# Kernel optimization log

Measured on AMD Instinct MI355X. Metric: run time of the kernel, lower is better.

## Reference

```python
import jax, jax.numpy as jnp
import numpy as np

ETA = 1.0
C_STAB = 0.1
SIGMA2 = 512.0  # RBF bandwidth, kernel_args['sigma2']
N_SAMPLE, S, D = 8192, 64, 512


def rbf_kernel(x, sigma2):
    # K[i,j] = exp(-||x_i - x_j||^2 / (2*sigma2)); x: [n, d] -> K: [n, n]
    sq = jnp.sum(x * x, axis=1)
    d2 = sq[:, None] + sq[None, :] - 2.0 * (x @ x.T)
    return jnp.exp(-d2 / (2.0 * sigma2))


def setup_inputs() -> dict:
    key = jax.random.key(0)
    k1, k2, k3 = jax.random.split(key, 3)
    return {
        "input_data": jax.random.normal(k1, (N_SAMPLE, D), dtype=jnp.float32),
        "weight": jax.random.normal(k2, (N_SAMPLE, S), dtype=jnp.float32),
        "inv_lambda_diag": jax.random.normal(k3, (S,), dtype=jnp.float32),
    }


def reference(input_data, weight, inv_lambda_diag):
    K = rbf_kernel(input_data, SIGMA2)          # [n, n]
    E = weight.T @ K                             # [s, n] : e_j for all samples at once
    # loss1 = sum_i e_i^T diag(inv_lambda) e_i, scaled
    loss1 = -jnp.sum(inv_lambda_diag[:, None] * E * E) / (2.0 * ETA ** 2)
    # loss2 = trace(W^T K W) = sum_{s,n} E[s,n] * W[n,s]
    loss2 = jnp.einsum("sn,ns->", E, weight) / (2.0 * ETA)
    L = loss1 + loss2
    return L + (C_STAB / 2.0) * jnp.square(L)
```

## Files before the change

### kernel.cpp

```cpp
#include <hip/hip_runtime.h>
#include <hip/hip_bf16.h>

typedef __bf16 bf16x8 __attribute__((ext_vector_type(8)));
typedef float f32x4 __attribute__((ext_vector_type(4)));
typedef long longx2 __attribute__((ext_vector_type(2)));
typedef int i32x8 __attribute__((ext_vector_type(8)));

#define N 8192
#define D 512
#define NS 64

#define XS_OFF 0
#define WT_OFF (4 * 1024 * 1024)
#define SQ_OFF (WT_OFF + 1024 * 1024)
#define EP_OFF (SQ_OFF + 32 * 1024)
#define SC_OFF (EP_OFF + 8 * 64 * 8192 * 4)

#define BAR() do { asm volatile("s_waitcnt lgkmcnt(0)" ::: "memory"); \
                   __builtin_amdgcn_s_barrier(); } while (0)

__global__ __launch_bounds__(256) void prep(const float* __restrict__ X,
                                            const float* __restrict__ W,
                                            unsigned char* __restrict__ Xs,
                                            float* __restrict__ sq,
                                            __bf16* __restrict__ WTs,
                                            float* __restrict__ Sacc) {
    __shared__ float T[64][65];
    int t = threadIdx.x;
    if (blockIdx.x == 0 && t == 0) {
        Sacc[0] = 0.f; Sacc[1] = 0.f; ((int*)Sacc)[2] = 0;
    }
    if (blockIdx.x < 2048) {
        int row = blockIdx.x * 4 + (t >> 6);
        int l = t & 63;
        const float* src = X + (size_t)row * D + l * 8;
        float4 v0 = *(const float4*)src;
        float4 v1 = *(const float4*)(src + 4);
        int w0 = __builtin_amdgcn_cvt_pk_fp8_f32(v0.x, v0.y, 0, false);
        w0     = __builtin_amdgcn_cvt_pk_fp8_f32(v0.z, v0.w, w0, true);
        int w1 = __builtin_amdgcn_cvt_pk_fp8_f32(v1.x, v1.y, 0, false);
        w1     = __builtin_amdgcn_cvt_pk_fp8_f32(v1.z, v1.w, w1, true);
        uint2 pk = make_uint2((unsigned)w0, (unsigned)w1);
        *(uint2*)(Xs + (size_t)row * 512 + l * 8) = pk;
        float acc = v0.x*v0.x + v0.y*v0.y + v0.z*v0.z + v0.w*v0.w
                  + v1.x*v1.x + v1.y*v1.y + v1.z*v1.z + v1.w*v1.w;
        for (int off = 32; off > 0; off >>= 1) acc += __shfl_down(acc, off);
        if (l == 0) sq[row] = acc;
    } else {
        int i0 = (blockIdx.x - 2048) * 64;
        for (int j = 0; j < 16; ++j) {
            int idx = t + 256 * j;
            T[idx & 63][idx >> 6] = W[(size_t)(i0 + (idx >> 6)) * NS + (idx & 63)];
        }
        __syncthreads();
        for (int h = 0; h < 2; ++h)
            for (int j = 0; j < 8; ++j) {
                int idx = t + 256 * j;
                int s = idx >> 5, il = idx & 31;
                WTs[(size_t)((i0 >> 5) + h) * 2048 + idx] = (__bf16)T[s][h * 32 + il];
            }
    }
}

__global__ __launch_bounds__(256, 2) void kpca_main(
        const unsigned char* __restrict__ Xs, const __bf16* __restrict__ WTs,
        const float* __restrict__ sq, float* __restrict__ Ep) {
    __shared__ __align__(16) unsigned char XiKT[18432];
    __shared__ __align__(16) unsigned char XnHi[3 * 16384];
    unsigned char* Xi = XiKT;
    __bf16* KT = (__bf16*)XiKT;

    const int t = threadIdx.x;
    const int w = t >> 6, l = t & 63;
    const int quad = l >> 4, l15 = l & 15;
    const int wm = w >> 1, wn = w & 1;
    const int n0 = blockIdx.x * 128;
    const int ic0 = blockIdx.y * 1024;

    union U8 { longx2 h[2]; i32x8 v; };

    U8 bc[4];
    {
        const unsigned char* Bb = Xs + (size_t)(n0 + wn * 64 + l15) * 512 + quad * 32;
        #pragma unroll
        for (int nt = 0; nt < 4; ++nt) {
            bc[nt].h[0] = *(const longx2*)(Bb + nt * 8192);
            bc[nt].h[1] = *(const longx2*)(Bb + nt * 8192 + 16);
        }
    }
    #pragma unroll 4
    for (int m = 0; m < 12; ++m) {
        int id = m * 256 + t;
        int c = id >> 10, rem = id & 1023;
        int r = rem >> 3, j = rem & 7;
        uint4 v = *(const uint4*)(Xs + (size_t)(n0 + r) * 512 + 128 + c * 128 + j * 16);
        *(uint4*)(XnHi + c * 16384 + r * 128 + ((j ^ (r & 7)) << 4)) = v;
    }
    float sqn_v[4];
    #pragma unroll
    for (int nt = 0; nt < 4; ++nt)
        sqn_v[nt] = sq[n0 + wn * 64 + nt * 16 + l15];

    f32x4 accE[4][2];
    #pragma unroll
    for (int st = 0; st < 4; ++st)
        for (int n2 = 0; n2 < 2; ++n2)
            accE[st][n2] = (f32x4){0.f, 0.f, 0.f, 0.f};

    const int rB = t >> 3;
    const int cB = (t & 7) * 16;
    const int swoff = (((t & 7) ^ ((t >> 3) & 7)) << 4);

    const int oswL = (((2 * quad)     ^ (l15 & 7)) << 4);
    const int oswH = (((2 * quad + 1) ^ (l15 & 7)) << 4);

    {
        const unsigned char* g = Xs + (size_t)(ic0 + rB) * 512 + cB;
        #pragma unroll
        for (int j = 0; j < 4; ++j)
            *(uint4*)(Xi + (size_t)(j * 32 + rB) * 128 + swoff) =
                *(const uint4*)(g + (size_t)j * 32 * 512);
    }

    uint4 q[4];

    for (int it = 0; it < 8; ++it) {
        const int i0 = ic0 + it * 128;
        f32x4 accG[4][4];
        #pragma unroll
        for (int mt = 0; mt < 4; ++mt)
            for (int nt = 0; nt < 4; ++nt)
                accG[mt][nt] = (f32x4){0.f, 0.f, 0.f, 0.f};

        if (it > 0) {
            BAR();
            #pragma unroll
            for (int j = 0; j < 4; ++j)
                *(uint4*)(Xi + (size_t)(j * 32 + rB) * 128 + swoff) = q[j];
        }

        #pragma unroll
        for (int ks = 0; ks < 4; ++ks) {
            if (ks < 3) {
                const unsigned char* g =
                    Xs + (size_t)(ic0 + it * 128 + rB) * 512 + (ks + 1) * 128 + cB;
                #pragma unroll
                for (int j = 0; j < 4; ++j)
                    q[j] = *(const uint4*)(g + (size_t)j * 32 * 512);
            }
            BAR();

            U8 a[4];
            const unsigned char* abase = Xi + (wm * 64 + l15) * 128;
            #pragma unroll
            for (int mt = 0; mt < 4; ++mt) {
                a[mt].h[0] = *(const longx2*)(abase + mt * 2048 + oswL);
                a[mt].h[1] = *(const longx2*)(abase + mt * 2048 + oswH);
            }
            __builtin_amdgcn_s_setprio(1);
            if (ks == 0) {
                #pragma unroll
                for (int nt = 0; nt < 4; ++nt)
                    #pragma unroll
                    for (int mt = 0; mt < 4; ++mt)
                        accG[mt][nt] = __builtin_amdgcn_mfma_scale_f32_16x16x128_f8f6f4(
                            a[mt].v, bc[nt].v, accG[mt][nt],
                            0, 0, 0, 0x7F7F7F7F, 0, 0x7F7F7F7F);
            } else {
                const unsigned char* bbase =
                    XnHi + (ks - 1) * 16384 + (wn * 64 + l15) * 128;
                #pragma unroll
                for (int nt = 0; nt < 4; ++nt) {
                    U8 bb;
                    bb.h[0] = *(const longx2*)(bbase + nt * 2048 + oswL);
                    bb.h[1] = *(const longx2*)(bbase + nt * 2048 + oswH);
                    #pragma unroll
                    for (int mt = 0; mt < 4; ++mt)
                        accG[mt][nt] = __builtin_amdgcn_mfma_scale_f32_16x16x128_f8f6f4(
                            a[mt].v, bb.v, accG[mt][nt],
                            0, 0, 0, 0x7F7F7F7F, 0, 0x7F7F7F7F);
                }
            }
            __builtin_amdgcn_s_setprio(0);

            if (ks < 3) {
                BAR();
                #pragma unroll
                for (int j = 0; j < 4; ++j)
                    *(uint4*)(Xi + (size_t)(j * 32 + rB) * 128 + swoff) = q[j];
            }
        }

        const __bf16* wslab = WTs + (size_t)(i0 >> 5) * 2048;

        auto write_pk = [&]() {
            #pragma unroll
            for (int mt = 0; mt < 4; ++mt) {
                f32x4 si = *(const f32x4*)(sq + i0 + wm * 64 + mt * 16 + quad * 4);
                #pragma unroll
                for (int nt = 0; nt < 4; ++nt) {
                    float sn = sqn_v[nt];
                    union { __bf16 h[4]; uint2 u; } u;
                    #pragma unroll
                    for (int r = 0; r < 4; ++r) {
                        float d2 = si[r] + sn - 2.0f * accG[mt][nt][r];
                        u.h[r] = (__bf16)__expf(d2 * -9.765625e-4f);
                    }
                    *(uint2*)(KT + (wn * 64 + nt * 16 + l15) * 72 + mt * 16 + quad * 4)
                        = u.u;
                }
            }
        };

        bf16x8 aw[2][4];
        #pragma unroll
        for (int kc2 = 0; kc2 < 2; ++kc2)
            for (int st = 0; st < 4; ++st)
                aw[kc2][st] = *(const bf16x8*)(wslab + kc2 * 2048 +
                                               (st * 16 + l15) * 32 + quad * 8);

        BAR();
        if (wm == 0) write_pk();
        BAR();
        #pragma unroll
        for (int kc2 = 0; kc2 < 2; ++kc2) {
            bf16x8 bk[2];
            for (int n2 = 0; n2 < 2; ++n2)
                bk[n2] = *(const bf16x8*)(KT + (w * 32 + n2 * 16 + l15) * 72 +
                                          kc2 * 32 + quad * 8);
            #pragma unroll
            for (int st = 0; st < 4; ++st)
                for (int n2 = 0; n2 < 2; ++n2)
                    accE[st][n2] = __builtin_amdgcn_mfma_f32_16x16x32_bf16(
                        aw[kc2][st], bk[n2], accE[st][n2], 0, 0, 0);
        }
        #pragma unroll
        for (int kc2 = 0; kc2 < 2; ++kc2)
            for (int st = 0; st < 4; ++st)
                aw[kc2][st] = *(const bf16x8*)(wslab + (kc2 + 2) * 2048 +
                                               (st * 16 + l15) * 32 + quad * 8);
        BAR();
        if (wm == 1) write_pk();
        if (it < 7) {
            const unsigned char* g =
                Xs + (size_t)(ic0 + (it + 1) * 128 + rB) * 512 + cB;
            #pragma unroll
            for (int j = 0; j < 4; ++j)
                q[j] = *(const uint4*)(g + (size_t)j * 32 * 512);
        }
        BAR();
        #pragma unroll
        for (int kc2 = 0; kc2 < 2; ++kc2) {
            bf16x8 bk[2];
            for (int n2 = 0; n2 < 2; ++n2)
                bk[n2] = *(const bf16x8*)(KT + (w * 32 + n2 * 16 + l15) * 72 +
                                          kc2 * 32 + quad * 8);
            #pragma unroll
            for (int st = 0; st < 4; ++st)
                for (int n2 = 0; n2 < 2; ++n2)
                    accE[st][n2] = __builtin_amdgcn_mfma_f32_16x16x32_bf16(
                        aw[kc2][st], bk[n2], accE[st][n2], 0, 0, 0);
        }
    }

    float* ep = Ep + (size_t)blockIdx.y * (NS * N);
    #pragma unroll
    for (int st = 0; st < 4; ++st)
        for (int n2 = 0; n2 < 2; ++n2)
            for (int r = 0; r < 4; ++r) {
                int s = st * 16 + quad * 4 + r;
                int n = n0 + w * 32 + n2 * 16 + l15;
                ep[(size_t)s * N + n] = accE[st][n2][r];
            }
}

__global__ __launch_bounds__(256) void loss_kernel(const float* __restrict__ Ep,
                                                   const __bf16* __restrict__ WTs,
                                                   const float* __restrict__ lam,
                                                   float* __restrict__ Sacc,
                                                   float* __restrict__ out) {
    int s = blockIdx.x >> 2;
    int nb = (blockIdx.x & 3) * 2048;
    int t = threadIdx.x;
    float a1 = 0.f, a2 = 0.f;
    for (int j = 0; j < 8; ++j) {
        int n = nb + t + j * 256;
        float e = 0.f;
        #pragma unroll
        for (int c = 0; c < 8; ++c)
            e += Ep[(size_t)c * (NS * N) + (size_t)s * N + n];
        a1 += e * e;
        a2 += e * (float)WTs[(size_t)(n >> 5) * 2048 + s * 32 + (n & 31)];
    }
    for (int off = 32; off > 0; off >>= 1) {
        a1 += __shfl_down(a1, off);
        a2 += __shfl_down(a2, off);
    }
    __shared__ float r1[4], r2[4];
    int wv = t >> 6, ln = t & 63;
    if (ln == 0) { r1[wv] = a1; r2[wv] = a2; }
    __syncthreads();
    if (t == 0) {
        atomicAdd(Sacc + 0, lam[s] * (r1[0] + r1[1] + r1[2] + r1[3]));
        atomicAdd(Sacc + 1, r2[0] + r2[1] + r2[2] + r2[3]);
        __threadfence();
        int prev = atomicAdd((int*)Sacc + 2, 1);
        if (prev == 255) {
            __threadfence();
            volatile float* vs = (volatile float*)Sacc;
            float L = 0.5f * (vs[1] - vs[0]);
            out[0] = L + 0.05f * L * L;
        }
    }
}

extern "C" void kernel_launch(void* const* d_in, const int* in_sizes, int n_in,
                              void* d_out, int out_size, void* d_ws, size_t ws_size,
                              hipStream_t stream) {
    const float* X   = (const float*)d_in[0];
    const float* W   = (const float*)d_in[1];
    const float* lam = (const float*)d_in[2];
    float* out = (float*)d_out;
    char* ws = (char*)d_ws;
    unsigned char* Xs = (unsigned char*)(ws + XS_OFF);
    __bf16* WTs = (__bf16*)(ws + WT_OFF);
    float* sq   = (float*)(ws + SQ_OFF);
    float* Ep   = (float*)(ws + EP_OFF);
    float* Sacc = (float*)(ws + SC_OFF);

    prep<<<2048 + 128, 256, 0, stream>>>(X, W, Xs, sq, WTs, Sacc);
    kpca_main<<<dim3(64, 8), 256, 0, stream>>>(Xs, WTs, sq, Ep);
    loss_kernel<<<256, 256, 0, stream>>>(Ep, WTs, lam, Sacc, out);
}
```

Baseline: 173.2 us.

## Stage full Xn tile in LDS and XOR-swizzle the K tile layout

The first 128-byte K-chunk of the Xn tile now goes to shared memory together with the other three, instead of being held in registers (bc). All four k-steps then share one code path. The bf16 K tile moves from a padded 72-element row stride to a 128-byte row with an XOR swizzle. This frees registers and aims to reduce LDS bank conflicts on the K writes and reads. In exchange, LDS use grows from about 66KB to 80KB per block, which may limit occupancy at two blocks per CU.

After: 165.4 us. 1.05x faster.

```diff
diff --git a/kernel.cpp b/kernel.cpp
--- a/kernel.cpp
+++ b/kernel.cpp
@@ -65,10 +65,9 @@
 __global__ __launch_bounds__(256, 2) void kpca_main(
         const unsigned char* __restrict__ Xs, const __bf16* __restrict__ WTs,
         const float* __restrict__ sq, float* __restrict__ Ep) {
-    __shared__ __align__(16) unsigned char XiKT[18432];
-    __shared__ __align__(16) unsigned char XnHi[3 * 16384];
+    __shared__ __align__(16) unsigned char XiKT[16384];
+    __shared__ __align__(16) unsigned char XnHi[4 * 16384];
     unsigned char* Xi = XiKT;
-    __bf16* KT = (__bf16*)XiKT;
 
     const int t = threadIdx.x;
     const int w = t >> 6, l = t & 63;
@@ -76,24 +75,16 @@
     const int wm = w >> 1, wn = w & 1;
     const int n0 = blockIdx.x * 128;
     const int ic0 = blockIdx.y * 1024;
+    const int sw7 = l15 & 7;
 
     union U8 { longx2 h[2]; i32x8 v; };
 
-    U8 bc[4];
-    {
-        const unsigned char* Bb = Xs + (size_t)(n0 + wn * 64 + l15) * 512 + quad * 32;
-        #pragma unroll
-        for (int nt = 0; nt < 4; ++nt) {
-            bc[nt].h[0] = *(const longx2*)(Bb + nt * 8192);
-            bc[nt].h[1] = *(const longx2*)(Bb + nt * 8192 + 16);
-        }
-    }
     #pragma unroll 4
-    for (int m = 0; m < 12; ++m) {
+    for (int m = 0; m < 16; ++m) {
         int id = m * 256 + t;
         int c = id >> 10, rem = id & 1023;
         int r = rem >> 3, j = rem & 7;
-        uint4 v = *(const uint4*)(Xs + (size_t)(n0 + r) * 512 + 128 + c * 128 + j * 16);
+        uint4 v = *(const uint4*)(Xs + (size_t)(n0 + r) * 512 + c * 128 + j * 16);
         *(uint4*)(XnHi + c * 16384 + r * 128 + ((j ^ (r & 7)) << 4)) = v;
     }
     float sqn_v[4];
@@ -111,8 +102,8 @@
     const int cB = (t & 7) * 16;
     const int swoff = (((t & 7) ^ ((t >> 3) & 7)) << 4);
 
-    const int oswL = (((2 * quad)     ^ (l15 & 7)) << 4);
-    const int oswH = (((2 * quad + 1) ^ (l15 & 7)) << 4);
+    const int oswL = (((2 * quad)     ^ sw7) << 4);
+    const int oswH = (((2 * quad + 1) ^ sw7) << 4);
 
     {
         const unsigned char* g = Xs + (size_t)(ic0 + rB) * 512 + cB;
@@ -157,29 +148,18 @@
                 a[mt].h[0] = *(const longx2*)(abase + mt * 2048 + oswL);
                 a[mt].h[1] = *(const longx2*)(abase + mt * 2048 + oswH);
             }
+            const unsigned char* bbase = XnHi + ks * 16384 + (wn * 64 + l15) * 128;
             __builtin_amdgcn_s_setprio(1);
-            if (ks == 0) {
+            #pragma unroll
+            for (int nt = 0; nt < 4; ++nt) {
+                U8 bb;
+                bb.h[0] = *(const longx2*)(bbase + nt * 2048 + oswL);
+                bb.h[1] = *(const longx2*)(bbase + nt * 2048 + oswH);
                 #pragma unroll
-                for (int nt = 0; nt < 4; ++nt)
-                    #pragma unroll
-                    for (int mt = 0; mt < 4; ++mt)
-                        accG[mt][nt] = __builtin_amdgcn_mfma_scale_f32_16x16x128_f8f6f4(
-                            a[mt].v, bc[nt].v, accG[mt][nt],
-                            0, 0, 0, 0x7F7F7F7F, 0, 0x7F7F7F7F);
-            } else {
-                const unsigned char* bbase =
-                    XnHi + (ks - 1) * 16384 + (wn * 64 + l15) * 128;
-                #pragma unroll
-                for (int nt = 0; nt < 4; ++nt) {
-                    U8 bb;
-                    bb.h[0] = *(const longx2*)(bbase + nt * 2048 + oswL);
-                    bb.h[1] = *(const longx2*)(bbase + nt * 2048 + oswH);
-                    #pragma unroll
-                    for (int mt = 0; mt < 4; ++mt)
-                        accG[mt][nt] = __builtin_amdgcn_mfma_scale_f32_16x16x128_f8f6f4(
-                            a[mt].v, bb.v, accG[mt][nt],
-                            0, 0, 0, 0x7F7F7F7F, 0, 0x7F7F7F7F);
-                }
+                for (int mt = 0; mt < 4; ++mt)
+                    accG[mt][nt] = __builtin_amdgcn_mfma_scale_f32_16x16x128_f8f6f4(
+                        a[mt].v, bb.v, accG[mt][nt],
+                        0, 0, 0, 0x7F7F7F7F, 0, 0x7F7F7F7F);
             }
             __builtin_amdgcn_s_setprio(0);
 
@@ -206,7 +186,9 @@
                         float d2 = si[r] + sn - 2.0f * accG[mt][nt][r];
                         u.h[r] = (__bf16)__expf(d2 * -9.765625e-4f);
                     }
-                    *(uint2*)(KT + (wn * 64 + nt * 16 + l15) * 72 + mt * 16 + quad * 4)
+                    int row = wn * 64 + nt * 16 + l15;
+                    int blk = mt * 2 + (quad >> 1);
+                    *(uint2*)(XiKT + row * 128 + ((blk ^ sw7) << 4) + (quad & 1) * 8)
                         = u.u;
                 }
             }
@@ -225,9 +207,11 @@
         #pragma unroll
         for (int kc2 = 0; kc2 < 2; ++kc2) {
             bf16x8 bk[2];
-            for (int n2 = 0; n2 < 2; ++n2)
-                bk[n2] = *(const bf16x8*)(KT + (w * 32 + n2 * 16 + l15) * 72 +
-                                          kc2 * 32 + quad * 8);
+            for (int n2 = 0; n2 < 2; ++n2) {
+                int row = w * 32 + n2 * 16 + l15;
+                bk[n2] = *(const bf16x8*)(XiKT + row * 128 +
+                                          (((kc2 * 4 + quad) ^ sw7) << 4));
+            }
             #pragma unroll
             for (int st = 0; st < 4; ++st)
                 for (int n2 = 0; n2 < 2; ++n2)
@@ -252,9 +236,11 @@
         #pragma unroll
         for (int kc2 = 0; kc2 < 2; ++kc2) {
             bf16x8 bk[2];
-            for (int n2 = 0; n2 < 2; ++n2)
-                bk[n2] = *(const bf16x8*)(KT + (w * 32 + n2 * 16 + l15) * 72 +
-                                          kc2 * 32 + quad * 8);
+            for (int n2 = 0; n2 < 2; ++n2) {
+                int row = w * 32 + n2 * 16 + l15;
+                bk[n2] = *(const bf16x8*)(XiKT + row * 128 +
+                                          (((kc2 * 4 + quad) ^ sw7) << 4));
+            }
             #pragma unroll
             for (int st = 0; st < 4; ++st)
                 for (int n2 = 0; n2 < 2; ++n2)
```
